# Optimization experiments

Hardware: AMD Instinct MI355X
Metric: run time of the kernel (lower is better)

Reference implementation:

```python
import jax, jax.numpy as jnp
import numpy as np

N = 100000
E = 3200000
IN_DIM = 256
HID = 128
HID2 = 64
K = 16


def setup_inputs() -> dict:
    key = jax.random.key(0)
    ks = jax.random.split(key, 12)
    x = jax.random.normal(ks[0], (N, IN_DIM), dtype=jnp.float32)
    edge_index = jax.random.randint(ks[1], (2, E), 0, N, dtype=jnp.int64)
    edge_weight = jax.random.uniform(ks[2], (E,), dtype=jnp.float32)
    s = lambda f: 1.0 / np.sqrt(f)
    W0 = jax.random.normal(ks[3], (IN_DIM, HID), dtype=jnp.float32) * s(IN_DIM)
    b0 = jnp.zeros((HID,), jnp.float32)
    P0w = jax.random.normal(ks[4], (IN_DIM, HID), dtype=jnp.float32) * s(IN_DIM)
    P0b = jnp.zeros((HID,), jnp.float32)
    W1 = jax.random.normal(ks[5], (HID, HID2), dtype=jnp.float32) * s(HID)
    b1 = jnp.zeros((HID2,), jnp.float32)
    P1w = jax.random.normal(ks[6], (HID, HID2), dtype=jnp.float32) * s(HID)
    P1b = jnp.zeros((HID2,), jnp.float32)
    W2 = jax.random.normal(ks[7], (HID2, K), dtype=jnp.float32) * s(HID2)
    b2 = jnp.zeros((K,), jnp.float32)
    return {"x": x, "edge_index": edge_index, "edge_weight": edge_weight,
            "W0": W0, "b0": b0, "P0w": P0w, "P0b": P0b,
            "W1": W1, "b1": b1, "P1w": P1w, "P1b": P1b,
            "W2": W2, "b2": b2}


def _gcn_norm(edge_index, edge_weight, n):
    # add self loops (weight 1), symmetric normalization per PyG gcn_norm
    loop = jnp.arange(n, dtype=edge_index.dtype)
    row = jnp.concatenate([edge_index[0], loop])
    col = jnp.concatenate([edge_index[1], loop])
    w = jnp.concatenate([edge_weight, jnp.ones((n,), edge_weight.dtype)])
    deg = jax.ops.segment_sum(w, col, num_segments=n)
    dinv = jnp.where(deg > 0, jax.lax.rsqrt(deg), 0.0)
    return row, col, dinv[row] * w * dinv[col]


def reference(x, edge_index, edge_weight, W0, b0, P0w, P0b, W1, b1, P1w, P1b, W2, b2):
    n = x.shape[0]
    row, col, nw = _gcn_norm(edge_index, edge_weight, n)

    def gcn(h, W, b):
        hW = h @ W  # transform first (PyG GCNConv), then scatter-aggregate
        agg = jax.ops.segment_sum(nw[:, None] * hW[row], col, num_segments=n)
        return agg + b

    # layer 0: skip is Linear(input_dim, hidden); dropout = identity (eval)
    h = jax.nn.selu(gcn(x, W0, b0) + (x @ P0w + P0b))
    # layer 1: skip is Linear(hidden, hidden//2)
    h = jax.nn.selu(gcn(h, W1, b1) + (h @ P1w + P1b))
    # layer 2: no skip, no dropout
    h = jax.nn.selu(gcn(h, W2, b2))
    return jax.nn.softmax(h, axis=-1)
```

## Files before the change

kernel.cpp:

```cpp
#include <hip/hip_runtime.h>
#include <hip/hip_fp16.h>
#include <cmath>

#define IN_DIM 256
#define HID 128
#define HID2 64
#define SB 256
#define NODES_PB 256
#define NBKT_MAX 448
#define BCAP 9216
#define CH 4096

struct __align__(8) EdgeP { int s; float w; };
union H4 { __half h[4]; uint2 u; };
union H2 { __half2 h2; uint u; };

using f16x8 = __attribute__((ext_vector_type(8))) _Float16;
using f32x4 = __attribute__((ext_vector_type(4))) float;

__device__ __forceinline__ float selu_f(float x) {
    const float scale = 1.0507009873554805f;
    const float alpha = 1.6732632423543772f;
    return x > 0.f ? scale * x : scale * alpha * expm1f(x);
}


__global__ void zero_ints(int* p, int n) {
    int i = blockIdx.x * blockDim.x + threadIdx.x;
    if (i < n) p[i] = 0;
}

__global__ void transpose_w(const float* __restrict__ B1, const float* __restrict__ B2,
                            __half* __restrict__ WT, int K, int C1, int C2) {
    int c = blockIdx.x;
    for (int k = threadIdx.x; k < K; k += blockDim.x) {
        float v = (c < C1) ? B1[(size_t)k * C1 + c] : B2[(size_t)k * C2 + (c - C1)];
        WT[(size_t)c * K + k] = __float2half(v);
    }
}

__global__ void deg_dinv(const EdgeP* __restrict__ ell, int* cnt, float* dinv, int n, int cap) {
    int wid = (blockIdx.x * blockDim.x + threadIdx.x) >> 6;
    int lane = threadIdx.x & 63;
    if (wid >= n) return;
    size_t base = (size_t)wid * cap;
    int len = min(cnt[wid], cap);
    float s = 0.f;
    for (int i = lane; i < len; i += 64) s += ell[base + i].w;
#pragma unroll
    for (int o = 32; o; o >>= 1) s += __shfl_xor(s, o);
    if (lane == 0) {
        dinv[wid] = rsqrtf(s + 1.0f);
        cnt[wid] = len;
    }
}

template <int PER>
__device__ __forceinline__ void wave0_excl_scan(const int* lds_in, int* lds_out, int nb, int tid) {
    if (tid < 64) {
        int r[PER];
        int sum = 0;
#pragma unroll
        for (int k = 0; k < PER; ++k) {
            int idx = tid * PER + k;
            int v = (idx < nb) ? lds_in[idx] : 0;
            r[k] = sum;
            sum += v;
        }
        int run = sum;
#pragma unroll
        for (int o = 1; o < 64; o <<= 1) {
            int t = __shfl_up(run, o);
            if (tid >= o) run += t;
        }
        int excl = run - sum;
#pragma unroll
        for (int k = 0; k < PER; ++k) {
            int idx = tid * PER + k;
            if (idx < nb) lds_out[idx] = excl + r[k];
        }
    }
}

__global__ __launch_bounds__(256) void bin_gemm0(
    const float* __restrict__ A, const __half* __restrict__ WT,
    const float* __restrict__ bias1, const float* __restrict__ bias2,
    __half* __restrict__ outA, float* __restrict__ outB, int M,
    const int* __restrict__ ei, const float* __restrict__ ew,
    int* cnt_or_bcur, EdgeP* __restrict__ dst_buf,
    int E, int cap, int epb, int sblocks, int nb, int mode) {
    const int tid = threadIdx.x;
    __shared__ __align__(16) char smem[48128];

    if ((int)blockIdx.x < sblocks) {
        int lo = blockIdx.x * epb;
        int hi = min(E, lo + epb);
        if (mode == 1) {
            int* hist = (int*)smem;
            int* off = hist + NBKT_MAX;
            int* cur = off + NBKT_MAX;
            int* gbase = cur + NBKT_MAX;
            int* sortedS = gbase + NBKT_MAX;
            float* sortedW = (float*)(sortedS + CH);
            short* smap = (short*)(sortedW + CH);
            for (int c0 = lo; c0 < hi; c0 += CH) {
                int cn = min(CH, hi - c0);
                for (int i = tid; i < nb; i += 256) hist[i] = 0;
                __syncthreads();
                for (int r = tid; r < cn; r += 256)
                    atomicAdd(&hist[ei[E + c0 + r] >> 8], 1);
                __syncthreads();
                wave0_excl_scan<7>(hist, off, nb, tid);
                __syncthreads();
                for (int b = tid; b < nb; b += 256) {
                    int h = hist[b];
                    gbase[b] = h ? atomicAdd(&cnt_or_bcur[b], h) : 0;
                    cur[b] = off[b];
                }
                __syncthreads();
                for (int r = tid; r < cn; r += 256) {
                    int e = c0 + r;
                    int d = ei[E + e];
                    int b = d >> 8;
                    int slot = atomicAdd(&cur[b], 1);
                    sortedS[slot] = (ei[e] << 8) | (d & 255);
                    sortedW[slot] = ew[e];
                    smap[slot] = (short)b;
                }
                __syncthreads();
                for (int i = tid; i < cn; i += 256) {
                    int b = smap[i];
                    int addr = gbase[b] + (i - off[b]);
                    if (addr < BCAP) {
                        EdgeP p; p.s = sortedS[i]; p.w = sortedW[i];
                        dst_buf[(size_t)b * BCAP + addr] = p;
                    }
                }
                __syncthreads();
            }
        } else {
            for (int base = lo; base < hi; base += 2048) {
                int r[8], c[8], pos[8];
                float wv[8];
#pragma unroll
                for (int j = 0; j < 8; ++j) {
                    int e = base + j * 256 + tid;
                    c[j] = -1;
                    if (e < hi) { r[j] = ei[e]; c[j] = ei[E + e]; wv[j] = ew[e]; }
                }
#pragma unroll
                for (int j = 0; j < 8; ++j)
                    if (c[j] >= 0) pos[j] = atomicAdd(&cnt_or_bcur[c[j]], 1);
#pragma unroll
                for (int j = 0; j < 8; ++j)
                    if (c[j] >= 0 && pos[j] < cap) {
                        EdgeP p; p.s = r[j]; p.w = wv[j];
                        dst_buf[(size_t)c[j] * cap + pos[j]] = p;
                    }
            }
        }
        return;
    }

    __half* sA16 = (__half*)smem;
    __half* sB16 = (__half*)(smem + 10240);
    const int bid = blockIdx.x - sblocks;
    const int m0 = (bid >> 1) * 128;
    const int n0 = (bid & 1) * 128;
    const int lane = tid & 63;
    const int wv = tid >> 6;
    const int wr = (wv >> 1) * 64;
    const int wc = (wv & 1) * 64;
    const int lr = lane & 15, lk = lane >> 4;

    f32x4 zero = {0.f, 0.f, 0.f, 0.f};
    f32x4 acc[4][4];
#pragma unroll
    for (int i = 0; i < 4; ++i)
#pragma unroll
        for (int j = 0; j < 4; ++j) acc[i][j] = zero;

    for (int k0 = 0; k0 < IN_DIM; k0 += 32) {
#pragma unroll
        for (int p = 0; p < 4; ++p) {
            int f4 = p * 256 + tid;
            int r = f4 >> 3;
            int kk = (f4 & 7) << 2;
            int row = m0 + r;
            float4 v = make_float4(0.f, 0.f, 0.f, 0.f);
            if (row < M) v = *(const float4*)(A + (size_t)row * IN_DIM + k0 + kk);
            H4 h;
            h.h[0] = __float2half(v.x); h.h[1] = __float2half(v.y);
            h.h[2] = __float2half(v.z); h.h[3] = __float2half(v.w);
            *(uint2*)&sA16[r * 40 + kk] = h.u;
        }
#pragma unroll
        for (int p = 0; p < 2; ++p) {
            int f = p * 256 + tid;
            int c = f >> 2;
            int kc = (f & 3) << 3;
            *(uint4*)&sB16[c * 40 + kc] =
                *(const uint4*)(WT + (size_t)(n0 + c) * IN_DIM + k0 + kc);
        }
        __syncthreads();
        f16x8 af[4], bf[4];
#pragma unroll
        for (int i = 0; i < 4; ++i)
            af[i] = *(const f16x8*)&sA16[(wr + i * 16 + lr) * 40 + lk * 8];
#pragma unroll
        for (int j = 0; j < 4; ++j)
            bf[j] = *(const f16x8*)&sB16[(wc + j * 16 + lr) * 40 + lk * 8];
#pragma unroll
        for (int i = 0; i < 4; ++i)
#pragma unroll
            for (int j = 0; j < 4; ++j)
                acc[i][j] = __builtin_amdgcn_mfma_f32_16x16x32_f16(af[i], bf[j], acc[i][j], 0, 0, 0);
        __syncthreads();
    }

    float bs[4];
    if (n0 != 0) {
#pragma unroll
        for (int j = 0; j < 4; ++j) {
            int c = wc + j * 16 + lr;
            bs[j] = bias1[c] + bias2[c];
        }
    }
#pragma unroll
    for (int i = 0; i < 4; ++i) {
        int rowb = m0 + wr + i * 16 + lk * 4;
#pragma unroll
        for (int j = 0; j < 4; ++j) {
            int col = wc + j * 16 + lr;
#pragma unroll
            for (int r = 0; r < 4; ++r) {
                int row = rowb + r;
                if (row < M) {
                    if (n0 == 0)
                        outA[(size_t)row * HID + col] = __float2half(acc[i][j][r]);
                    else
                        outB[(size_t)row * HID + col] = acc[i][j][r] + bs[j];
                }
            }
        }
    }
}

__global__ __launch_bounds__(256) void bucket_build(
    const EdgeP* __restrict__ recs, const int* __restrict__ bcur,
    EdgeP* __restrict__ ell, int* __restrict__ cnt, float* __restrict__ dinv,
    int n, int cap) {
    __shared__ int lcnt[NODES_PB];
    __shared__ float ldeg[NODES_PB];
    __shared__ int chist[NODES_PB];
    __shared__ int coff[NODES_PB];
    __shared__ int ccur[NODES_PB];
    __shared__ __align__(8) int sortedS[CH];
    __shared__ float sortedW[CH];
    __shared__ unsigned char cmap[CH];
    int b = blockIdx.x, tid = threadIdx.x;
    lcnt[tid] = 0;
    ldeg[tid] = 0.f;
    __syncthreads();
    int m = min(bcur[b], BCAP);
    const EdgeP* rbase = recs + (size_t)b * BCAP;
    for (int c0 = 0; c0 < m; c0 += CH) {
        int cn = min(CH, m - c0);
        chist[tid] = 0;
        __syncthreads();
        for (int i = tid; i < cn; i += 256) {
            EdgeP p = rbase[c0 + i];
            int dl = p.s & 255;
            atomicAdd(&chist[dl], 1);
            atomicAdd(&ldeg[dl], p.w);
        }
        __syncthreads();
        wave0_excl_scan<4>(chist, coff, NODES_PB, tid);
        __syncthreads();
        ccur[tid] = coff[tid];
        __syncthreads();
        for (int i = tid; i < cn; i += 256) {
            EdgeP p = rbase[c0 + i];
            int dl = p.s & 255;
            int slot = atomicAdd(&ccur[dl], 1);
            sortedS[slot] = p.s >> 8;
            sortedW[slot] = p.w;
            cmap[slot] = (unsigned char)dl;
        }
        __syncthreads();
        for (int i = tid; i < cn; i += 256) {
            int dl = cmap[i];
            int rank = lcnt[dl] + (i - coff[dl]);
            if (rank < cap) {
                EdgeP q; q.s = sortedS[i]; q.w = sortedW[i];
                ell[((size_t)(b * NODES_PB + dl)) * cap + rank] = q;
            }
        }
        __syncthreads();
        lcnt[tid] += chist[tid];
        __syncthreads();
    }
    int v = b * NODES_PB + tid;
    if (v < n) {
        cnt[v] = min(lcnt[tid], cap);
        dinv[v] = rsqrtf(ldeg[tid] + 1.0f);
    }
}

__global__ __launch_bounds__(256) void gemm1_fused(
    const float* __restrict__ A, const __half* __restrict__ WT,
    const float* __restrict__ bias1, const float* __restrict__ bias2,
    __half* __restrict__ outA, float* __restrict__ outB, int M) {
    const int tid = threadIdx.x;
    __shared__ __align__(16) __half sA16[128 * 40];
    __shared__ __align__(16) __half sB16[128 * 40];
    const int m0 = blockIdx.x * 128;
    const int lane = tid & 63;
    const int wv = tid >> 6;
    const int wr = (wv >> 1) * 64;
    const int wc = (wv & 1) * 64;
    const int lr = lane & 15, lk = lane >> 4;

    f32x4 zero = {0.f, 0.f, 0.f, 0.f};
    f32x4 acc[4][4];
#pragma unroll
    for (int i = 0; i < 4; ++i)
#pragma unroll
        for (int j = 0; j < 4; ++j) acc[i][j] = zero;

    for (int k0 = 0; k0 < HID; k0 += 32) {
#pragma unroll
        for (int p = 0; p < 4; ++p) {
            int f4 = p * 256 + tid;
            int r = f4 >> 3;
            int kk = (f4 & 7) << 2;
            int row = m0 + r;
            float4 v = make_float4(0.f, 0.f, 0.f, 0.f);
            if (row < M) v = *(const float4*)(A + (size_t)row * HID + k0 + kk);
            H4 h;
            h.h[0] = __float2half(v.x); h.h[1] = __float2half(v.y);
            h.h[2] = __float2half(v.z); h.h[3] = __float2half(v.w);
            *(uint2*)&sA16[r * 40 + kk] = h.u;
        }
#pragma unroll
        for (int p = 0; p < 2; ++p) {
            int f = p * 256 + tid;
            int c = f >> 2;
            int kc = (f & 3) << 3;
            *(uint4*)&sB16[c * 40 + kc] =
                *(const uint4*)(WT + (size_t)c * HID + k0 + kc);
        }
        __syncthreads();
        f16x8 af[4], bf[4];
#pragma unroll
        for (int i = 0; i < 4; ++i)
            af[i] = *(const f16x8*)&sA16[(wr + i * 16 + lr) * 40 + lk * 8];
#pragma unroll
        for (int j = 0; j < 4; ++j)
            bf[j] = *(const f16x8*)&sB16[(wc + j * 16 + lr) * 40 + lk * 8];
#pragma unroll
        for (int i = 0; i < 4; ++i)
#pragma unroll
            for (int j = 0; j < 4; ++j)
                acc[i][j] = __builtin_amdgcn_mfma_f32_16x16x32_f16(af[i], bf[j], acc[i][j], 0, 0, 0);
        __syncthreads();
    }

    float bs[4];
    if (wc != 0) {
#pragma unroll
        for (int j = 0; j < 4; ++j) {
            int c = wc + j * 16 + lr - HID2;
            bs[j] = bias1[c] + bias2[c];
        }
    }
#pragma unroll
    for (int i = 0; i < 4; ++i) {
        int rowb = m0 + wr + i * 16 + lk * 4;
#pragma unroll
        for (int j = 0; j < 4; ++j) {
            int col = wc + j * 16 + lr;
#pragma unroll
            for (int r = 0; r < 4; ++r) {
                int row = rowb + r;
                if (row < M) {
                    if (wc == 0)
                        outA[(size_t)row * HID2 + col] = __float2half(acc[i][j][r]);
                    else
                        outB[(size_t)row * HID2 + (col - HID2)] = acc[i][j][r] + bs[j];
                }
            }
        }
    }
}

__global__ __launch_bounds__(256) void aggregate128(
    const __half* __restrict__ hW, float* __restrict__ S,
    const float* __restrict__ dinv, const int* __restrict__ cnt,
    const EdgeP* __restrict__ ell, int cap, int n) {
    int v = (blockIdx.x * 256 + threadIdx.x) >> 6;
    int lane = threadIdx.x & 63;
    if (v >= n) return;
    float di = dinv[v];
    float2 sv = *(const float2*)&S[(size_t)v * HID + lane * 2];
    H2 selfh; selfh.u = *(const uint*)&hW[(size_t)v * HID + lane * 2];
    float2 selff = __half22float2(selfh.h2);
    float selfx = sv.x + di * di * selff.x;
    float selfy = sv.y + di * di * selff.y;

    size_t base = (size_t)v * cap;
    int len = cnt[v];
    float ax[4] = {0.f, 0.f, 0.f, 0.f};
    float ay[4] = {0.f, 0.f, 0.f, 0.f};
    int i = 0;
    for (; i + 8 <= len; i += 8) {
        EdgeP p[8];
        float dv[8];
        uint h[8];
#pragma unroll
        for (int j = 0; j < 8; ++j) p[j] = ell[base + i + j];
#pragma unroll
        for (int j = 0; j < 8; ++j) {
            dv[j] = dinv[p[j].s];
            h[j] = *(const uint*)&hW[(size_t)p[j].s * HID + lane * 2];
        }
#pragma unroll
        for (int j = 0; j < 8; ++j) {
            float t = dv[j] * p[j].w;
            H2 hh; hh.u = h[j];
            float2 hf = __half22float2(hh.h2);
            ax[j & 3] = fmaf(t, hf.x, ax[j & 3]);
            ay[j & 3] = fmaf(t, hf.y, ay[j & 3]);
        }
    }
    for (; i < len; ++i) {
        EdgeP p = ell[base + i];
        float t = dinv[p.s] * p.w;
        H2 hh; hh.u = *(const uint*)&hW[(size_t)p.s * HID + lane * 2];
        float2 hf = __half22float2(hh.h2);
        ax[0] = fmaf(t, hf.x, ax[0]);
        ay[0] = fmaf(t, hf.y, ay[0]);
    }
    float sx = selfx + di * ((ax[0] + ax[1]) + (ax[2] + ax[3]));
    float sy = selfy + di * ((ay[0] + ay[1]) + (ay[2] + ay[3]));
    *(float2*)&S[(size_t)v * HID + lane * 2] = make_float2(selu_f(sx), selu_f(sy));
}

__global__ __launch_bounds__(256) void agg64_gemm2(
    const __half* __restrict__ hW, const float* __restrict__ S,
    const float* __restrict__ dinv, const int* __restrict__ cnt,
    const EdgeP* __restrict__ ell, int cap,
    const float* __restrict__ W2, __half* __restrict__ out16, int n) {
    __shared__ float sW[64 * 16];
    __shared__ float sh[4][64];
    int tid = threadIdx.x;
#pragma unroll
    for (int i = 0; i < 4; ++i) sW[i * 256 + tid] = W2[i * 256 + tid];

    int g = tid >> 6, f = tid & 63;
    int v = blockIdx.x * 4 + g;
    if (v < n) {
        float di = dinv[v];
        float self = S[(size_t)v * 64 + f] + di * di * __half2float(hW[(size_t)v * 64 + f]);
        size_t base = (size_t)v * cap;
        int len = cnt[v];
        float a[4] = {0.f, 0.f, 0.f, 0.f};
        int i = 0;
        for (; i + 8 <= len; i += 8) {
            EdgeP p[8];
            float dv[8];
            __half hv[8];
#pragma unroll
            for (int j = 0; j < 8; ++j) p[j] = ell[base + i + j];
#pragma unroll
            for (int j = 0; j < 8; ++j) {
                dv[j] = dinv[p[j].s];
                hv[j] = hW[(size_t)p[j].s * 64 + f];
            }
#pragma unroll
            for (int j = 0; j < 8; ++j)
                a[j & 3] = fmaf(dv[j] * p[j].w, __half2float(hv[j]), a[j & 3]);
        }
        for (; i < len; ++i) {
            EdgeP p = ell[base + i];
            a[0] = fmaf(dinv[p.s] * p.w, __half2float(hW[(size_t)p.s * 64 + f]), a[0]);
        }
        sh[g][f] = selu_f(self + di * ((a[0] + a[1]) + (a[2] + a[3])));
    }
    __syncthreads();
    if (v < n && f < 16) {
        float acc = 0.f;
#pragma unroll
        for (int k = 0; k < 64; ++k) acc = fmaf(sh[g][k], sW[k * 16 + f], acc);
        out16[(size_t)v * 16 + f] = __float2half(acc);
    }
}

__global__ __launch_bounds__(256) void agg_softmax(
    const __half* __restrict__ hW, const float* __restrict__ b2,
    const float* __restrict__ dinv, const int* __restrict__ cnt,
    const EdgeP* __restrict__ ell, int cap,
    float* __restrict__ out, int n) {
    int tid = threadIdx.x;
    int g = tid >> 4, f = tid & 15;
    int v = blockIdx.x * 16 + g;
    if (v >= n) return;
    float di = dinv[v];
    float acc = b2[f] + di * di * __half2float(hW[(size_t)v * 16 + f]);
    size_t base = (size_t)v * cap;
    int len = cnt[v];
    float a[4] = {0.f, 0.f, 0.f, 0.f};
    int i = 0;
    for (; i + 4 <= len; i += 4) {
        EdgeP p[4];
        float dv[4];
        __half hv[4];
#pragma unroll
        for (int j = 0; j < 4; ++j) p[j] = ell[base + i + j];
#pragma unroll
        for (int j = 0; j < 4; ++j) {
            dv[j] = dinv[p[j].s];
            hv[j] = hW[(size_t)p[j].s * 16 + f];
        }
#pragma unroll
        for (int j = 0; j < 4; ++j)
            a[j] = fmaf(dv[j] * p[j].w, __half2float(hv[j]), a[j]);
    }
    for (; i < len; ++i) {
        EdgeP p = ell[base + i];
        a[0] = fmaf(dinv[p.s] * p.w, __half2float(hW[(size_t)p.s * 16 + f]), a[0]);
    }
    acc += di * ((a[0] + a[1]) + (a[2] + a[3]));
    acc = selu_f(acc);
    float m = acc;
    m = fmaxf(m, __shfl_xor(m, 1));
    m = fmaxf(m, __shfl_xor(m, 2));
    m = fmaxf(m, __shfl_xor(m, 4));
    m = fmaxf(m, __shfl_xor(m, 8));
    float ex = expf(acc - m);
    float sm = ex;
    sm += __shfl_xor(sm, 1);
    sm += __shfl_xor(sm, 2);
    sm += __shfl_xor(sm, 4);
    sm += __shfl_xor(sm, 8);
    out[(size_t)v * 16 + f] = ex / sm;
}

extern "C" void kernel_launch(void* const* d_in, const int* in_sizes, int n_in,
                              void* d_out, int out_size, void* d_ws, size_t ws_size,
                              hipStream_t stream) {
    const float* x = (const float*)d_in[0];
    const int* ei = (const int*)d_in[1];
    const float* ew = (const float*)d_in[2];
    const float* W0 = (const float*)d_in[3];
    const float* b0 = (const float*)d_in[4];
    const float* P0w = (const float*)d_in[5];
    const float* P0b = (const float*)d_in[6];
    const float* W1 = (const float*)d_in[7];
    const float* b1 = (const float*)d_in[8];
    const float* P1w = (const float*)d_in[9];
    const float* P1b = (const float*)d_in[10];
    const float* W2 = (const float*)d_in[11];
    const float* b2 = (const float*)d_in[12];
    float* out = (float*)d_out;
    const int n = in_sizes[0] / IN_DIM;
    const int E = in_sizes[2];
    const int NB = (n + NODES_PB - 1) / NODES_PB;

    auto al = [](size_t b) { return (b + 255) & ~(size_t)255; };
    size_t oCnt = 0;
    size_t oDinv = oCnt + al((size_t)n * 4);
    size_t oBcur = oDinv + al((size_t)n * 4);
    size_t oWT0 = oBcur + al((size_t)NBKT_MAX * 4);
    size_t oWT1 = oWT0 + al((size_t)IN_DIM * (HID * 2) * 2);
    size_t oA = oWT1 + al((size_t)HID * HID * 2);
    size_t oB = oA + al((size_t)n * HID * 2);
    size_t oEll = oB + al((size_t)n * HID * 4);
    size_t szEll96 = al((size_t)n * 96 * 8);
    size_t szEll80 = al((size_t)n * 80 * 8);
    size_t szRec = al((size_t)NB * BCAP * 8);
    size_t szCD = al((size_t)n * HID2 * 4) + al((size_t)n * 16 * 2);
    size_t szR = szRec > szCD ? szRec : szCD;

    int cap;
    int mode;
    if (NB <= NBKT_MAX && oEll + szEll96 + szR <= ws_size) { cap = 96; mode = 1; }
    else if (oEll + szEll96 + szCD <= ws_size) { cap = 96; mode = 0; }
    else { cap = 80; mode = 0; }

    char* base = (char*)d_ws;
    int* cnt = (int*)(base + oCnt);
    float* dinv = (float*)(base + oDinv);
    int* bcur = (int*)(base + oBcur);
    __half* WT0 = (__half*)(base + oWT0);
    __half* WT1 = (__half*)(base + oWT1);
    __half* bufA = (__half*)(base + oA);
    float* bufB = (float*)(base + oB);
    EdgeP* ell = (EdgeP*)(base + oEll);
    size_t oR = oEll + (cap == 96 ? szEll96 : szEll80);
    EdgeP* recs = (EdgeP*)(base + oR);
    float* bufC = (float*)(base + oR);
    __half* bufD = (__half*)(base + oR + al((size_t)n * HID2 * 4));

    int gx = (n + 127) / 128;
    int gemmBlocks = gx * 2;
    int epb = (E + SB - 1) / SB;

    transpose_w<<<2 * HID, 128, 0, stream>>>(W0, P0w, WT0, IN_DIM, HID, HID);
    transpose_w<<<HID, 128, 0, stream>>>(W1, P1w, WT1, HID, HID2, HID2);

    if (mode == 1) {
        zero_ints<<<(NBKT_MAX + 255) / 256, 256, 0, stream>>>(bcur, NBKT_MAX);
        bin_gemm0<<<SB + gemmBlocks, 256, 0, stream>>>(
            x, WT0, b0, P0b, bufA, bufB, n, ei, ew, bcur, recs,
            E, cap, epb, SB, NB, 1);
        bucket_build<<<NB, NODES_PB, 0, stream>>>(recs, bcur, ell, cnt, dinv, n, cap);
    } else {
        zero_ints<<<(n + 255) / 256, 256, 0, stream>>>(cnt, n);
        bin_gemm0<<<SB + gemmBlocks, 256, 0, stream>>>(
            x, WT0, b0, P0b, bufA, bufB, n, ei, ew, cnt, ell,
            E, cap, epb, SB, NB, 0);
        int nbW = (n * 64 + 255) / 256;
        deg_dinv<<<nbW, 256, 0, stream>>>(ell, cnt, dinv, n, cap);
    }

    aggregate128<<<(n * 64 + 255) / 256, 256, 0, stream>>>(bufA, bufB, dinv, cnt, ell, cap, n);

    gemm1_fused<<<gx, 256, 0, stream>>>(bufB, WT1, b1, P1b, bufA, bufC, n);

    agg64_gemm2<<<(n + 3) / 4, 256, 0, stream>>>(bufA, bufC, dinv, cnt, ell, cap, W2, bufD, n);
    agg_softmax<<<(n + 15) / 16, 256, 0, stream>>>(bufD, b2, dinv, cnt, ell, cap, out, n);
}
```

Before: 495.7 us.

## Shrink binning LDS footprint with per-block global reservation and smaller chunks

The edge-binning path now reserves global bucket space once per block with a full histogram pass, then processes smaller 2048-edge chunks. It packs the high bucket bit into the source key so the map array can be bytes. Shared memory drops from about 48KB to about 25KB, which lets more blocks fit per CU, and the number of scatter blocks is doubled. In exchange the edge destinations are read one extra time, and the packing assumes source index fits in 17 bits and bucket count fits in 9 bits.

```diff
diff --git a/kernel.cpp b/kernel.cpp
--- a/kernel.cpp
+++ b/kernel.cpp
@@ -5,11 +5,13 @@
 #define IN_DIM 256
 #define HID 128
 #define HID2 64
-#define SB 256
+#define SB 512
 #define NODES_PB 256
 #define NBKT_MAX 448
 #define BCAP 9216
+#define CHB 2048
 #define CH 4096
+#define SMEM_BIN (4 * NBKT_MAX * 4 + CHB * 9)
 
 struct __align__(8) EdgeP { int s; float w; };
 union H4 { __half h[4]; uint2 u; };
@@ -90,52 +92,63 @@
     int* cnt_or_bcur, EdgeP* __restrict__ dst_buf,
     int E, int cap, int epb, int sblocks, int nb, int mode) {
     const int tid = threadIdx.x;
-    __shared__ __align__(16) char smem[48128];
+    __shared__ __align__(16) char smem[SMEM_BIN];
 
     if ((int)blockIdx.x < sblocks) {
         int lo = blockIdx.x * epb;
         int hi = min(E, lo + epb);
         if (mode == 1) {
-            int* hist = (int*)smem;
-            int* off = hist + NBKT_MAX;
-            int* cur = off + NBKT_MAX;
-            int* gbase = cur + NBKT_MAX;
-            int* sortedS = gbase + NBKT_MAX;
-            float* sortedW = (float*)(sortedS + CH);
-            short* smap = (short*)(sortedW + CH);
-            for (int c0 = lo; c0 < hi; c0 += CH) {
-                int cn = min(CH, hi - c0);
-                for (int i = tid; i < nb; i += 256) hist[i] = 0;
+            int* gwcur = (int*)smem;
+            int* chist = gwcur + NBKT_MAX;
+            int* coff = chist + NBKT_MAX;
+            int* ccur = coff + NBKT_MAX;
+            int* sortedS = ccur + NBKT_MAX;
+            float* sortedW = (float*)(sortedS + CHB);
+            unsigned char* smap = (unsigned char*)(sortedW + CHB);
+
+            for (int i = tid; i < nb; i += 256) chist[i] = 0;
+            __syncthreads();
+            for (int e = lo + tid; e < hi; e += 256)
+                atomicAdd(&chist[ei[E + e] >> 8], 1);
+            __syncthreads();
+            for (int b = tid; b < nb; b += 256) {
+                int h = chist[b];
+                gwcur[b] = h ? atomicAdd(&cnt_or_bcur[b], h) : 0;
+            }
+            __syncthreads();
+
+            for (int c0 = lo; c0 < hi; c0 += CHB) {
+                int cn = min(CHB, hi - c0);
+                for (int i = tid; i < nb; i += 256) chist[i] = 0;
                 __syncthreads();
                 for (int r = tid; r < cn; r += 256)
-                    atomicAdd(&hist[ei[E + c0 + r] >> 8], 1);
+                    atomicAdd(&chist[ei[E + c0 + r] >> 8], 1);
                 __syncthreads();
-                wave0_excl_scan<7>(hist, off, nb, tid);
+                wave0_excl_scan<7>(chist, coff, nb, tid);
                 __syncthreads();
-                for (int b = tid; b < nb; b += 256) {
-                    int h = hist[b];
-                    gbase[b] = h ? atomicAdd(&cnt_or_bcur[b], h) : 0;
-                    cur[b] = off[b];
-                }
+                for (int b = tid; b < nb; b += 256) ccur[b] = coff[b];
                 __syncthreads();
                 for (int r = tid; r < cn; r += 256) {
                     int e = c0 + r;
                     int d = ei[E + e];
                     int b = d >> 8;
-                    int slot = atomicAdd(&cur[b], 1);
-                    sortedS[slot] = (ei[e] << 8) | (d & 255);
+                    int slot = atomicAdd(&ccur[b], 1);
+                    sortedS[slot] = (ei[e] << 8) | (d & 255) | ((b >> 8) << 25);
                     sortedW[slot] = ew[e];
-                    smap[slot] = (short)b;
+                    smap[slot] = (unsigned char)(b & 255);
                 }
                 __syncthreads();
                 for (int i = tid; i < cn; i += 256) {
-                    int b = smap[i];
-                    int addr = gbase[b] + (i - off[b]);
+                    int key = sortedS[i];
+                    int b = smap[i] | (((key >> 25) & 1) << 8);
+                    int addr = gwcur[b] + (i - coff[b]);
                     if (addr < BCAP) {
-                        EdgeP p; p.s = sortedS[i]; p.w = sortedW[i];
+                        EdgeP p; p.s = key & 0x01FFFFFF; p.w = sortedW[i];
                         dst_buf[(size_t)b * BCAP + addr] = p;
                     }
                 }
+                __syncthreads();
+                for (int b = tid; b < nb; b += 256) gwcur[b] += chist[b];
                 __syncthreads();
             }
         } else {
```

Measured after the change: 507.4 us. +2.4%, slower.
